# Performance work log

Hardware: AMD Instinct MI355X
Metric: run time of the kernel (lower is better)

The kernel has to match this reference:

```python
import jax, jax.numpy as jnp
import numpy as np

K = 255
L = 1.0 / K
W = L / 2.5
MU = (L * (jnp.arange(K, dtype=jnp.float32) + 0.5))  # [K]


def soft_hist(x):
    # x: [B, H, W] -> [B, K] soft histogram (mean of sigmoid-window memberships)
    B = x.shape[0]
    N = x.shape[1] * x.shape[2]
    xf = x.reshape(B, 1, -1)                      # [B, 1, N]
    d = xf - MU[None, :, None]                    # [B, K, N]
    pj = jax.nn.sigmoid((d + L / 2) / W) - jax.nn.sigmoid((d - L / 2) / W)
    return pj.sum(axis=2) / N                     # [B, K]


def emd(x, y):
    # matmul with lower-triangular ones == cumulative sum along bins
    cdf_x = jnp.cumsum(x, axis=1)
    cdf_y = jnp.cumsum(y, axis=1)
    return jnp.sum(jnp.square(cdf_x - cdf_y), axis=1)  # [B]


def setup_inputs() -> dict:
    key = jax.random.key(0)
    k1, k2 = jax.random.split(key)
    img = jax.random.uniform(k1, (8, 3, 256, 256), dtype=jnp.float32)
    img_t = jax.random.uniform(k2, (8, 3, 256, 256), dtype=jnp.float32)
    return {"img": img, "img_t": img_t}


def reference(img, img_t):
    r, g, b = img[:, 0], img[:, 1], img[:, 2]
    r_t, g_t, b_t = img_t[:, 0], img_t[:, 1], img_t[:, 2]
    r_hist = soft_hist(r)
    g_hist = soft_hist(g)
    b_hist = soft_hist(b)
    r_t_hist = soft_hist(r_t)  # computed but unused, faithful to original (bug: earth(r_hist, r_hist))
    g_t_hist = soft_hist(g_t)
    b_t_hist = soft_hist(b_t)
    loss = emd(r_hist, r_hist) + emd(g_hist, g_t_hist) + emd(b_hist, b_t_hist)
    return loss  # [B]
```

## Files before the change

### kernel.cpp

```cpp
#include <hip/hip_runtime.h>


#define PADF 64
#define CNTF4 1056

__device__ __forceinline__ float fsigmoid(float z) {
    return __builtin_amdgcn_rcpf(1.0f + __expf(-z));
}

__global__ __launch_bounds__(512) void fine_hist_kernel(
    const float* __restrict__ img, const float* __restrict__ img_t,
    uint4* __restrict__ part)
{
    const int blk = blockIdx.x;
    const int h   = blk >> 4;
    const int s   = blk & 15;
    const int b   = h >> 2;
    const int ch  = 1 + ((h >> 1) & 1);
    const float* src = (h & 1) ? img_t : img;
    const float4* base = (const float4*)(src + (size_t)(b * 3 + ch) * 65536u
                                             + (size_t)s * 4096u);

    __shared__ unsigned hist[4096];
    uint4* h4 = (uint4*)hist;
    h4[threadIdx.x]       = make_uint4(0u, 0u, 0u, 0u);
    h4[threadIdx.x + 512] = make_uint4(0u, 0u, 0u, 0u);
    __syncthreads();

    #pragma unroll
    for (int r = 0; r < 2; ++r) {
        const float4 v = base[threadIdx.x + 512 * r];
        int j0 = (int)(v.x * 4080.0f);
        int j1 = (int)(v.y * 4080.0f);
        int j2 = (int)(v.z * 4080.0f);
        int j3 = (int)(v.w * 4080.0f);
        j0 = j0 < 0 ? 0 : (j0 > 4079 ? 4079 : j0);
        j1 = j1 < 0 ? 0 : (j1 > 4079 ? 4079 : j1);
        j2 = j2 < 0 ? 0 : (j2 > 4079 ? 4079 : j2);
        j3 = j3 < 0 ? 0 : (j3 > 4079 ? 4079 : j3);
        atomicAdd(&hist[j0], 1u);
        atomicAdd(&hist[j1], 1u);
        atomicAdd(&hist[j2], 1u);
        atomicAdd(&hist[j3], 1u);
    }
    __syncthreads();

    if (threadIdx.x < 256) {
        const int t = threadIdx.x;
        const uint4 q0 = h4[4 * t + 0];
        const uint4 q1 = h4[4 * t + 1];
        const uint4 q2 = h4[4 * t + 2];
        const uint4 q3 = h4[4 * t + 3];
        uint4 o;
        o.x = q0.x | (q0.y << 8) | (q0.z << 16) | (q0.w << 24);
        o.y = q1.x | (q1.y << 8) | (q1.z << 16) | (q1.w << 24);
        o.z = q2.x | (q2.y << 8) | (q2.z << 16) | (q2.w << 24);
        o.w = q3.x | (q3.y << 8) | (q3.z << 16) | (q3.w << 24);
        part[(size_t)blk * 256u + t] = o;
    }
}

__global__ __launch_bounds__(256) void cdf_kernel(
    const uint4* __restrict__ part, float* __restrict__ cdf)
{
    const int h = blockIdx.x;
    const int k = threadIdx.x;

    __shared__ float4 cnt4[CNTF4];
    __shared__ float  coarse[256];
    __shared__ float4 sgt4[32];
    __shared__ float  s0sh;

    float* cn = (float*)cnt4;

    if (k < 128)
        ((float*)sgt4)[k] = fsigmoid((2.5f / 16.0f) * ((float)k + 0.5f) - 10.0f);

    unsigned a[16];
    #pragma unroll
    for (int i = 0; i < 16; ++i) a[i] = 0u;
    const uint4* p0 = part + (size_t)h * 16u * 256u + k;
    #pragma unroll
    for (int p = 0; p < 16; ++p) {
        const uint4 u = p0[p * 256];
        a[0]  += u.x & 255u; a[1]  += (u.x >> 8) & 255u;
        a[2]  += (u.x >> 16) & 255u; a[3]  += u.x >> 24;
        a[4]  += u.y & 255u; a[5]  += (u.y >> 8) & 255u;
        a[6]  += (u.y >> 16) & 255u; a[7]  += u.y >> 24;
        a[8]  += u.z & 255u; a[9]  += (u.z >> 8) & 255u;
        a[10] += (u.z >> 16) & 255u; a[11] += u.z >> 24;
        a[12] += u.w & 255u; a[13] += (u.w >> 8) & 255u;
        a[14] += (u.w >> 16) & 255u; a[15] += u.w >> 24;
    }
    float f[16], fs = 0.0f;
    #pragma unroll
    for (int i = 0; i < 16; ++i) { f[i] = (float)a[i]; fs += f[i]; }
    coarse[k] = fs;

    #pragma unroll
    for (int r = 0; r < 4; ++r) {
        const int rr = (r + k) & 3;
        cnt4[16 + 4 * k + rr] =
            make_float4(f[4 * rr], f[4 * rr + 1], f[4 * rr + 2], f[4 * rr + 3]);
    }
    if (k < PADF) cn[k] = 0.0f;
    if (k < PADF) cn[PADF + 4096 + k] = 0.0f;
    __syncthreads();

    if (k < 64) {
        float s0p = cn[PADF + k] * fsigmoid((2.5f / 16.0f) * ((float)k + 0.5f));
        #pragma unroll
        for (int off = 32; off; off >>= 1) s0p += __shfl_down(s0p, off);
        if (k == 0) s0sh = s0p;
    }
    __syncthreads();

    for (int off = 1; off < 256; off <<= 1) {
        const float v = (k + off < 256) ? coarse[k + off] : 0.0f;
        __syncthreads();
        coarse[k] += v;
        __syncthreads();
    }

    float t = 0.0f;
    #pragma unroll
    for (int c = 0; c < 32; ++c) {
        const int cc = (c + k) & 31;
        const float4 av = cnt4[4 * k + 4 + cc];
        const float4 wv = sgt4[cc];
        t += av.x * wv.x + av.y * wv.y + av.z * wv.z + av.w * wv.w;
    }
    const float ones = (k + 5 < 256) ? coarse[k + 5] : 0.0f;
    const float S0   = s0sh + coarse[4];

    cdf[h * 256 + k] = (k <= 254) ? (S0 - t - ones) * (1.0f / 65536.0f) : 0.0f;
}

__global__ __launch_bounds__(256) void emd_kernel(
    const float* __restrict__ cdf, float* __restrict__ out)
{
    const int b = blockIdx.x;
    const int k = threadIdx.x;
    const float* c0 = cdf + (size_t)(b * 4 + 0) * 256u;
    const float* c1 = cdf + (size_t)(b * 4 + 1) * 256u;
    const float* c2 = cdf + (size_t)(b * 4 + 2) * 256u;
    const float* c3 = cdf + (size_t)(b * 4 + 3) * 256u;

    const float dg = c0[k] - c1[k];
    const float db = c2[k] - c3[k];
    float v = dg * dg + db * db;
    #pragma unroll
    for (int off = 32; off; off >>= 1) v += __shfl_down(v, off);
    __shared__ float red[4];
    if ((k & 63) == 0) red[k >> 6] = v;
    __syncthreads();
    if (k == 0) out[b] = red[0] + red[1] + red[2] + red[3];
}

extern "C" void kernel_launch(void* const* d_in, const int* in_sizes, int n_in,
                              void* d_out, int out_size, void* d_ws, size_t ws_size,
                              hipStream_t stream)
{
    const float* img   = (const float*)d_in[0];
    const float* img_t = (const float*)d_in[1];
    float* out = (float*)d_out;

    uint4* part = (uint4*)d_ws;
    float* cdfb = (float*)((char*)d_ws + (size_t)512 * 4096u);

    hipLaunchKernelGGL(fine_hist_kernel, dim3(512), dim3(512), 0, stream,
                       img, img_t, part);
    hipLaunchKernelGGL(cdf_kernel, dim3(32), dim3(256), 0, stream,
                       part, cdfb);
    hipLaunchKernelGGL(emd_kernel, dim3(8), dim3(256), 0, stream,
                       cdfb, out);
}
```

Measured before the change: 67.91 us.

## Fuse CDF and EMD kernels, double histogram grid to 1024 blocks

The fine histogram kernel now runs 1024 blocks of 2048 pixels each instead of 512 blocks of 4096, which raises parallelism across the GPU. The CDF and EMD kernels are merged into one 512-thread kernel where each block computes both CDFs of a channel pair and atomically adds the squared difference into the output. This drops one kernel launch and the intermediate CDF round trip. In exchange, the partial histograms written to global memory double in volume, and the output must be zeroed inside the first kernel.

```diff
diff --git a/kernel.cpp b/kernel.cpp
--- a/kernel.cpp
+++ b/kernel.cpp
@@ -10,16 +10,18 @@
 
 __global__ __launch_bounds__(512) void fine_hist_kernel(
     const float* __restrict__ img, const float* __restrict__ img_t,
-    uint4* __restrict__ part)
+    uint2* __restrict__ part, float* __restrict__ out)
 {
     const int blk = blockIdx.x;
-    const int h   = blk >> 4;
-    const int s   = blk & 15;
+    const int h   = blk >> 5;
+    const int s   = blk & 31;
     const int b   = h >> 2;
     const int ch  = 1 + ((h >> 1) & 1);
     const float* src = (h & 1) ? img_t : img;
     const float4* base = (const float4*)(src + (size_t)(b * 3 + ch) * 65536u
-                                             + (size_t)s * 4096u);
+                                             + (size_t)s * 2048u);
+
+    if (blk == 0 && threadIdx.x < 8) out[threadIdx.x] = 0.0f;
 
     __shared__ unsigned hist[4096];
     uint4* h4 = (uint4*)hist;
@@ -27,62 +29,59 @@
     h4[threadIdx.x + 512] = make_uint4(0u, 0u, 0u, 0u);
     __syncthreads();
 
-    #pragma unroll
-    for (int r = 0; r < 2; ++r) {
-        const float4 v = base[threadIdx.x + 512 * r];
-        int j0 = (int)(v.x * 4080.0f);
-        int j1 = (int)(v.y * 4080.0f);
-        int j2 = (int)(v.z * 4080.0f);
-        int j3 = (int)(v.w * 4080.0f);
-        j0 = j0 < 0 ? 0 : (j0 > 4079 ? 4079 : j0);
-        j1 = j1 < 0 ? 0 : (j1 > 4079 ? 4079 : j1);
-        j2 = j2 < 0 ? 0 : (j2 > 4079 ? 4079 : j2);
-        j3 = j3 < 0 ? 0 : (j3 > 4079 ? 4079 : j3);
-        atomicAdd(&hist[j0], 1u);
-        atomicAdd(&hist[j1], 1u);
-        atomicAdd(&hist[j2], 1u);
-        atomicAdd(&hist[j3], 1u);
-    }
+    const float4 v = base[threadIdx.x];
+    int j0 = (int)(v.x * 4080.0f);
+    int j1 = (int)(v.y * 4080.0f);
+    int j2 = (int)(v.z * 4080.0f);
+    int j3 = (int)(v.w * 4080.0f);
+    j0 = j0 < 0 ? 0 : (j0 > 4079 ? 4079 : j0);
+    j1 = j1 < 0 ? 0 : (j1 > 4079 ? 4079 : j1);
+    j2 = j2 < 0 ? 0 : (j2 > 4079 ? 4079 : j2);
+    j3 = j3 < 0 ? 0 : (j3 > 4079 ? 4079 : j3);
+    atomicAdd(&hist[j0], 1u);
+    atomicAdd(&hist[j1], 1u);
+    atomicAdd(&hist[j2], 1u);
+    atomicAdd(&hist[j3], 1u);
     __syncthreads();
 
-    if (threadIdx.x < 256) {
-        const int t = threadIdx.x;
-        const uint4 q0 = h4[4 * t + 0];
-        const uint4 q1 = h4[4 * t + 1];
-        const uint4 q2 = h4[4 * t + 2];
-        const uint4 q3 = h4[4 * t + 3];
-        uint4 o;
-        o.x = q0.x | (q0.y << 8) | (q0.z << 16) | (q0.w << 24);
-        o.y = q1.x | (q1.y << 8) | (q1.z << 16) | (q1.w << 24);
-        o.z = q2.x | (q2.y << 8) | (q2.z << 16) | (q2.w << 24);
-        o.w = q3.x | (q3.y << 8) | (q3.z << 16) | (q3.w << 24);
-        part[(size_t)blk * 256u + t] = o;
-    }
+    const uint4 q0 = h4[2 * threadIdx.x];
+    const uint4 q1 = h4[2 * threadIdx.x + 1];
+    uint2 o;
+    o.x = q0.x | (q0.y << 8) | (q0.z << 16) | (q0.w << 24);
+    o.y = q1.x | (q1.y << 8) | (q1.z << 16) | (q1.w << 24);
+    part[(size_t)blk * 512u + threadIdx.x] = o;
 }
 
-__global__ __launch_bounds__(256) void cdf_kernel(
-    const uint4* __restrict__ part, float* __restrict__ cdf)
+__global__ __launch_bounds__(512) void cdf_emd_kernel(
+    const uint4* __restrict__ part, float* __restrict__ out)
 {
-    const int h = blockIdx.x;
-    const int k = threadIdx.x;
+    const int p   = blockIdx.x;
+    const int b   = p >> 1;
+    const int c   = p & 1;
+    const int tid = threadIdx.x;
+    const int sg  = tid >> 8;
+    const int k   = tid & 255;
+    const int h   = 4 * b + 2 * c + sg;
 
-    __shared__ float4 cnt4[CNTF4];
-    __shared__ float  coarse[256];
+    __shared__ float4 cnt4[2][CNTF4];
+    __shared__ float  coarse[2][256];
     __shared__ float4 sgt4[32];
-    __shared__ float  s0sh;
+    __shared__ float  s0sh[2];
+    __shared__ float  cdfs[2][256];
+    __shared__ float  lred[4];
 
-    float* cn = (float*)cnt4;
+    float* cn = (float*)cnt4[sg];
 
-    if (k < 128)
-        ((float*)sgt4)[k] = fsigmoid((2.5f / 16.0f) * ((float)k + 0.5f) - 10.0f);
+    if (tid < 128)
+        ((float*)sgt4)[tid] = fsigmoid((2.5f / 16.0f) * ((float)tid + 0.5f) - 10.0f);
 
     unsigned a[16];
     #pragma unroll
     for (int i = 0; i < 16; ++i) a[i] = 0u;
-    const uint4* p0 = part + (size_t)h * 16u * 256u + k;
+    const uint4* p0 = part + (size_t)h * 32u * 256u + k;
     #pragma unroll
-    for (int p = 0; p < 16; ++p) {
-        const uint4 u = p0[p * 256];
+    for (int q = 0; q < 32; ++q) {
+        const uint4 u = p0[q * 256];
         a[0]  += u.x & 255u; a[1]  += (u.x >> 8) & 255u;
         a[2]  += (u.x >> 16) & 255u; a[3]  += u.x >> 24;
         a[4]  += u.y & 255u; a[5]  += (u.y >> 8) & 255u;
@@ -95,12 +94,12 @@
     float f[16], fs = 0.0f;
     #pragma unroll
     for (int i = 0; i < 16; ++i) { f[i] = (float)a[i]; fs += f[i]; }
-    coarse[k] = fs;
+    coarse[sg][k] = fs;
 
     #pragma unroll
     for (int r = 0; r < 4; ++r) {
         const int rr = (r + k) & 3;
-        cnt4[16 + 4 * k + rr] =
+        cnt4[sg][16 + 4 * k + rr] =
             make_float4(f[4 * rr], f[4 * rr + 1], f[4 * rr + 2], f[4 * rr + 3]);
     }
     if (k < PADF) cn[k] = 0.0f;
@@ -111,50 +110,39 @@
         float s0p = cn[PADF + k] * fsigmoid((2.5f / 16.0f) * ((float)k + 0.5f));
         #pragma unroll
         for (int off = 32; off; off >>= 1) s0p += __shfl_down(s0p, off);
-        if (k == 0) s0sh = s0p;
+        if (k == 0) s0sh[sg] = s0p;
     }
-    __syncthreads();
 
     for (int off = 1; off < 256; off <<= 1) {
-        const float v = (k + off < 256) ? coarse[k + off] : 0.0f;
+        const float v = (k + off < 256) ? coarse[sg][k + off] : 0.0f;
         __syncthreads();
-        coarse[k] += v;
+        coarse[sg][k] += v;
         __syncthreads();
     }
 
     float t = 0.0f;
     #pragma unroll
-    for (int c = 0; c < 32; ++c) {
-        const int cc = (c + k) & 31;
-        const float4 av = cnt4[4 * k + 4 + cc];
+    for (int cc0 = 0; cc0 < 32; ++cc0) {
+        const int cc = (cc0 + k) & 31;
+        const float4 av = cnt4[sg][4 * k + 4 + cc];
         const float4 wv = sgt4[cc];
         t += av.x * wv.x + av.y * wv.y + av.z * wv.z + av.w * wv.w;
     }
-    const float ones = (k + 5 < 256) ? coarse[k + 5] : 0.0f;
-    const float S0   = s0sh + coarse[4];
+    const float ones = (k + 5 < 256) ? coarse[sg][k + 5] : 0.0f;
+    const float S0   = s0sh[sg] + coarse[sg][4];
 
-    cdf[h * 256 + k] = (k <= 254) ? (S0 - t - ones) * (1.0f / 65536.0f) : 0.0f;
-}
+    cdfs[sg][k] = (k <= 254) ? (S0 - t - ones) * (1.0f / 65536.0f) : 0.0f;
+    __syncthreads();
 
-__global__ __launch_bounds__(256) void emd_kernel(
-    const float* __restrict__ cdf, float* __restrict__ out)
-{
-    const int b = blockIdx.x;
-    const int k = threadIdx.x;
-    const float* c0 = cdf + (size_t)(b * 4 + 0) * 256u;
-    const float* c1 = cdf + (size_t)(b * 4 + 1) * 256u;
-    const float* c2 = cdf + (size_t)(b * 4 + 2) * 256u;
-    const float* c3 = cdf + (size_t)(b * 4 + 3) * 256u;
-
-    const float dg = c0[k] - c1[k];
-    const float db = c2[k] - c3[k];
-    float v = dg * dg + db * db;
-    #pragma unroll
-    for (int off = 32; off; off >>= 1) v += __shfl_down(v, off);
-    __shared__ float red[4];
-    if ((k & 63) == 0) red[k >> 6] = v;
+    if (tid < 256) {
+        const float d = cdfs[0][tid] - cdfs[1][tid];
+        float v = d * d;
+        #pragma unroll
+        for (int off = 32; off; off >>= 1) v += __shfl_down(v, off);
+        if ((tid & 63) == 0) lred[tid >> 6] = v;
+    }
     __syncthreads();
-    if (k == 0) out[b] = red[0] + red[1] + red[2] + red[3];
+    if (tid == 0) atomicAdd(&out[b], lred[0] + lred[1] + lred[2] + lred[3]);
 }
 
 extern "C" void kernel_launch(void* const* d_in, const int* in_sizes, int n_in,
@@ -165,13 +153,10 @@
     const float* img_t = (const float*)d_in[1];
     float* out = (float*)d_out;
 
-    uint4* part = (uint4*)d_ws;
-    float* cdfb = (float*)((char*)d_ws + (size_t)512 * 4096u);
+    uint2* part = (uint2*)d_ws;
 
-    hipLaunchKernelGGL(fine_hist_kernel, dim3(512), dim3(512), 0, stream,
-                       img, img_t, part);
-    hipLaunchKernelGGL(cdf_kernel, dim3(32), dim3(256), 0, stream,
-                       part, cdfb);
-    hipLaunchKernelGGL(emd_kernel, dim3(8), dim3(256), 0, stream,
-                       cdfb, out);
+    hipLaunchKernelGGL(fine_hist_kernel, dim3(1024), dim3(512), 0, stream,
+                       img, img_t, part, out);
+    hipLaunchKernelGGL(cdf_emd_kernel, dim3(16), dim3(512), 0, stream,
+                       (const uint4*)part, out);
 }
```

New measurement: 69.63 us. +2.5%, slower.
